# Performance work log

Hardware: AMD Instinct MI355X
Metric: run time of the kernel (lower is better)

Reference implementation:

```python
import jax, jax.numpy as jnp
import numpy as np

EMBED = 1024
HEADS = 16
HEAD_DIM = EMBED // HEADS
B, S = 2, 2048


def setup_inputs() -> dict:
    key = jax.random.key(0)
    ks = jax.random.split(key, 9)
    std = 1.0 / np.sqrt(EMBED)
    mk = lambda k: jax.random.uniform(k, (EMBED, EMBED), jnp.float32, -std, std)
    bk = lambda k: jax.random.uniform(k, (EMBED,), jnp.float32, -std, std)
    return {
        "x": jax.random.normal(ks[0], (B, S, EMBED), jnp.float32),
        "Wq": mk(ks[1]), "bq": bk(ks[2]),
        "Wk": mk(ks[3]), "bk": bk(ks[4]),
        "Wv": mk(ks[5]), "bv": bk(ks[6]),
        "Wo": mk(ks[7]), "bo": bk(ks[8]),
    }


def reference(x, Wq, bq, Wk, bk, Wv, bv, Wo, bo):
    b, s, _ = x.shape
    scale = HEAD_DIM ** -0.5
    # Linear layers: y = x @ W^T + b (torch nn.Linear convention)
    def heads(W, bias):
        y = jnp.einsum('bse,fe->bsf', x, W) + bias
        return y.reshape(b, s, HEADS, HEAD_DIM).transpose(0, 2, 1, 3)  # [b,h,s,d]
    Q, K, V = heads(Wq, bq), heads(Wk, bk), heads(Wv, bv)
    scores = jnp.einsum('bhqd,bhkd->bhqk', Q, K) * scale
    attn = jax.nn.softmax(scores, axis=-1)
    out = jnp.einsum('bhqk,bhkd->bhqd', attn, V)
    out = out.transpose(0, 2, 1, 3).reshape(b, s, EMBED)
    return jnp.einsum('bse,fe->bsf', out, Wo) + bo
```

## Files before the change

kernel.cpp:

```cpp
#include <hip/hip_runtime.h>
#include <hip/hip_bf16.h>
#include <cstddef>

#define SEQ   2048
#define EMB   1024
#define NHEAD 16
#define HDIM  64
#define BATCH 2
#define MROWS (BATCH * SEQ)
#define BH_STRIDE (SEQ * HDIM)
#define CSC_F 0.180336874f

typedef __attribute__((ext_vector_type(8))) short frag_ab;
typedef __attribute__((ext_vector_type(4))) float frag_cd;

#define GLOBAL_AS __attribute__((address_space(1)))
#define LDS_AS    __attribute__((address_space(3)))

__device__ __forceinline__ unsigned short f2bf(float f) {
    unsigned u = __float_as_uint(f);
    u += 0x7FFF + ((u >> 16) & 1);
    return (unsigned short)(u >> 16);
}
__device__ __forceinline__ unsigned short f2bf_trunc(float f) {
    return (unsigned short)(__float_as_uint(f) >> 16);
}
__device__ __forceinline__ void gld16(const unsigned short* g, unsigned short* l) {
    __builtin_amdgcn_global_load_lds((GLOBAL_AS const unsigned int*)g,
                                     (LDS_AS unsigned int*)l, 16, 0, 0);
}

__global__ __launch_bounds__(256) void cvt_all(const float* __restrict__ x,
                                               const float* __restrict__ Wq,
                                               const float* __restrict__ Wk,
                                               const float* __restrict__ Wv,
                                               unsigned short* __restrict__ xb,
                                               unsigned short* __restrict__ wqkv) {
    size_t e = ((size_t)blockIdx.x * 256 + threadIdx.x) * 8;
    const float* s;
    unsigned short* d;
    float sc = 1.0f;
    const size_t NX = (size_t)MROWS * EMB;
    const size_t NW = (size_t)EMB * EMB;
    if (e < NX) { s = x + e; d = xb + e; }
    else if (e < NX + NW)     { s = Wq + (e - NX);          d = wqkv + (e - NX); sc = CSC_F; }
    else if (e < NX + 2 * NW) { s = Wk + (e - NX - NW);     d = wqkv + (e - NX); }
    else                      { s = Wv + (e - NX - 2 * NW); d = wqkv + (e - NX); }
    float4 f0 = *(const float4*)s;
    float4 f1 = *(const float4*)(s + 4);
    ushort4 lo, hi;
    lo.x = f2bf(f0.x * sc); lo.y = f2bf(f0.y * sc); lo.z = f2bf(f0.z * sc); lo.w = f2bf(f0.w * sc);
    hi.x = f2bf(f1.x * sc); hi.y = f2bf(f1.y * sc); hi.z = f2bf(f1.z * sc); hi.w = f2bf(f1.w * sc);
    *(ushort4*)d = lo;
    *(ushort4*)(d + 4) = hi;
}

__global__ __launch_bounds__(256) void cvt_bf16(const float* __restrict__ s,
                                                unsigned short* __restrict__ d, int n) {
    int i = (blockIdx.x * 256 + threadIdx.x) * 8;
    if (i >= n) return;
    float4 f0 = *(const float4*)&s[i];
    float4 f1 = *(const float4*)&s[i + 4];
    ushort4 lo, hi;
    lo.x = f2bf(f0.x); lo.y = f2bf(f0.y); lo.z = f2bf(f0.z); lo.w = f2bf(f0.w);
    hi.x = f2bf(f1.x); hi.y = f2bf(f1.y); hi.z = f2bf(f1.z); hi.w = f2bf(f1.w);
    *(ushort4*)&d[i] = lo;
    *(ushort4*)&d[i + 4] = hi;
}

template <bool QKV>
__global__ __launch_bounds__(256, 3) void gemm128(const unsigned short* __restrict__ A,
                                                  const unsigned short* __restrict__ W0,
                                                  const unsigned short* __restrict__ W1,
                                                  const unsigned short* __restrict__ W2,
                                                  const float* __restrict__ b0,
                                                  const float* __restrict__ b1,
                                                  const float* __restrict__ b2,
                                                  void* __restrict__ o0,
                                                  void* __restrict__ o1,
                                                  void* __restrict__ o2) {
    constexpr int K = EMB;
    __shared__ __align__(16) unsigned short SB[16384];
    unsigned short* As = SB;
    unsigned short* Bs = SB + 8192;

    const int bidx = blockIdx.x;
    const int g8 = bidx & 7, t = bidx >> 3;
    const int my = g8 * 4 + (t & 3);
    const int mx = QKV ? ((t >> 2) & 7) : (t >> 2);
    const int z = QKV ? (t >> 5) : 0;

    const unsigned short* W = (z == 0) ? W0 : (z == 1) ? W1 : W2;
    const float* bias = (z == 0) ? b0 : (z == 1) ? b1 : b2;
    void* outv = (z == 0) ? o0 : (z == 1) ? o1 : o2;

    const int m0 = my * 128;
    const int n0 = mx * 128;
    const int tid = threadIdx.x;
    const int lane = tid & 63, w = tid >> 6;
    const int wr = w >> 1, wc = w & 1;
    const int lm = lane & 15, lq = lane >> 4;

    const int cs = (((tid & 7) ^ ((tid >> 3) & 7)) << 3);
    const int sx = lm & 7;

    frag_cd acc[4][4];
#pragma unroll
    for (int mt = 0; mt < 4; ++mt)
#pragma unroll
        for (int nt = 0; nt < 4; ++nt) acc[mt][nt] = (frag_cd){0.f, 0.f, 0.f, 0.f};

    for (int k0 = 0; k0 < K; k0 += 64) {
#pragma unroll
        for (int it = 0; it < 4; ++it) {
            int flat = (it * 256 + tid) * 8;
            int r = flat >> 6;
            gld16(&A[(size_t)(m0 + r) * K + k0 + cs], &As[flat]);
        }
#pragma unroll
        for (int it = 0; it < 4; ++it) {
            int flat = (it * 256 + tid) * 8;
            int r = flat >> 6;
            gld16(&W[(size_t)(n0 + r) * K + k0 + cs], &Bs[flat]);
        }
        __syncthreads();

#pragma unroll
        for (int kk = 0; kk < 2; ++kk) {
            frag_ab af[4], bf[4];
#pragma unroll
            for (int mt = 0; mt < 4; ++mt)
                af[mt] = *(const frag_ab*)&As[(wr * 64 + mt * 16 + lm) * 64
                                              + (((kk * 4 + lq) ^ sx) << 3)];
#pragma unroll
            for (int nt = 0; nt < 4; ++nt)
                bf[nt] = *(const frag_ab*)&Bs[(wc * 64 + nt * 16 + lm) * 64
                                              + (((kk * 4 + lq) ^ sx) << 3)];
#pragma unroll
            for (int mt = 0; mt < 4; ++mt)
#pragma unroll
                for (int nt = 0; nt < 4; ++nt)
                    acc[mt][nt] = __builtin_amdgcn_mfma_f32_16x16x32_bf16(
                        af[mt], bf[nt], acc[mt][nt], 0, 0, 0);
        }
        __syncthreads();
    }

    const float bscale = (QKV && z == 0) ? CSC_F : 1.0f;
    if (!QKV) {
#pragma unroll
        for (int mt = 0; mt < 4; ++mt)
#pragma unroll
            for (int nt = 0; nt < 4; ++nt) {
                int col = n0 + wc * 64 + nt * 16 + lm;
                float bv = bias[col];
#pragma unroll
                for (int r = 0; r < 4; ++r) {
                    int row = m0 + wr * 64 + mt * 16 + lq * 4 + r;
                    ((float*)outv)[(size_t)row * EMB + col] = acc[mt][nt][r] + bv;
                }
            }
    } else {
#pragma unroll
        for (int mt = 0; mt < 4; ++mt)
#pragma unroll
            for (int nt = 0; nt < 4; ++nt) {
                int col = n0 + wc * 64 + nt * 16 + lm;
                float bv = bias[col] * bscale;
#pragma unroll
                for (int r = 0; r < 4; ++r) {
                    unsigned short o = f2bf(acc[mt][nt][r] + bv);
                    int l, pos;
                    if (z < 2) {
                        l = wc * 16 + (wr * 4 + mt) * 2 + (nt >> 1);
                        pos = ((nt * 2 + (lm >> 3)) & 3) * 128 + (lq * 4 + r) * 8 + (lm & 7);
                    } else {
                        l = wc * 16 + (wr * 2 + (mt >> 1)) * 4 + nt;
                        pos = ((mt & 1) * 2 + (lq >> 1)) * 128 + lm * 8 + (lq & 1) * 4 + r;
                    }
                    SB[l * 512 + pos] = o;
                }
            }
        __syncthreads();

        unsigned short* out = (unsigned short*)outv;
        const int b = m0 >> 11;
        const int hb = n0 >> 6;
        const int sg16 = (m0 & (SEQ - 1)) >> 4;
        const int sb32 = (m0 & (SEQ - 1)) >> 5;
#pragma unroll
        for (int it = 0; it < 8; ++it) {
            int cl = it * 4 + w;
            uint4 v = *(const uint4*)&SB[cl * 512 + lane * 8];
            size_t chunk;
            if (z < 2) {
                int h = cl >> 4, sg = (cl >> 1) & 7, dh = cl & 1;
                chunk = ((size_t)(b * NHEAD + hb + h) * 128 + sg16 + sg) * 2 + dh;
            } else {
                int h = cl >> 4, sb = (cl >> 2) & 3, dq = cl & 3;
                chunk = ((size_t)(b * NHEAD + hb + h) * 64 + sb32 + sb) * 4 + dq;
            }
            *(uint4*)&out[chunk * 512 + lane * 8] = v;
        }
    }
}

#define PSTRIDE 72

struct KVset { frag_ab k[4][2]; frag_ab v[2][4]; };

__device__ __forceinline__ void kv_load(const unsigned short* __restrict__ Kb,
                                        const unsigned short* __restrict__ Vb,
                                        int j, int lane, KVset& s) {
    const int kg = j >> 4, jb = j >> 5;
#pragma unroll
    for (int c = 0; c < 4; ++c) {
        s.k[c][0] = *(const frag_ab*)&Kb[(((kg + c) * 2 + 0) * 64 + lane) * 8];
        s.k[c][1] = *(const frag_ab*)&Kb[(((kg + c) * 2 + 1) * 64 + lane) * 8];
    }
#pragma unroll
    for (int jj = 0; jj < 2; ++jj)
#pragma unroll
        for (int dt = 0; dt < 4; ++dt)
            s.v[jj][dt] = *(const frag_ab*)&Vb[(((jb + jj) * 4 + dt) * 64 + lane) * 8];
}

__device__ __forceinline__ void attn_step(const KVset& s, const frag_ab (&qf)[2][2],
                                          const frag_ab& vone,
                                          frag_cd (&oa)[2][4], frag_cd (&oc)[2],
                                          unsigned short* __restrict__ Pw,
                                          int lm, int lq) {
    const frag_cd z = (frag_cd){0.f, 0.f, 0.f, 0.f};
#pragma unroll
    for (int c = 0; c < 4; ++c) {
#pragma unroll
        for (int qi = 0; qi < 2; ++qi) {
            frag_cd sc = __builtin_amdgcn_mfma_f32_16x16x32_bf16(qf[qi][0], s.k[c][0], z, 0, 0, 0);
            sc = __builtin_amdgcn_mfma_f32_16x16x32_bf16(qf[qi][1], s.k[c][1], sc, 0, 0, 0);
#pragma unroll
            for (int r = 0; r < 4; ++r) {
                float p = __builtin_amdgcn_exp2f(sc[r]);
                Pw[(qi * 16 + lq * 4 + r) * PSTRIDE + c * 16 + lm] = f2bf_trunc(p);
            }
        }
    }

    frag_ab pf[2][2];
#pragma unroll
    for (int qi = 0; qi < 2; ++qi) {
        pf[qi][0] = *(const frag_ab*)&Pw[(qi * 16 + lm) * PSTRIDE + lq * 8];
        pf[qi][1] = *(const frag_ab*)&Pw[(qi * 16 + lm) * PSTRIDE + 32 + lq * 8];
        oc[qi] = __builtin_amdgcn_mfma_f32_16x16x32_bf16(pf[qi][0], vone, oc[qi], 0, 0, 0);
        oc[qi] = __builtin_amdgcn_mfma_f32_16x16x32_bf16(pf[qi][1], vone, oc[qi], 0, 0, 0);
    }

#pragma unroll
    for (int dt = 0; dt < 4; ++dt)
#pragma unroll
        for (int qi = 0; qi < 2; ++qi) {
            oa[qi][dt] = __builtin_amdgcn_mfma_f32_16x16x32_bf16(pf[qi][0], s.v[0][dt], oa[qi][dt], 0, 0, 0);
            oa[qi][dt] = __builtin_amdgcn_mfma_f32_16x16x32_bf16(pf[qi][1], s.v[1][dt], oa[qi][dt], 0, 0, 0);
        }
}

__global__ __launch_bounds__(256, 2) void attn_fused(const unsigned short* __restrict__ Q,
                                                     const unsigned short* __restrict__ Kf,
                                                     const unsigned short* __restrict__ Vf,
                                                     unsigned short* __restrict__ O) {
    const int bidx = blockIdx.x;
    const int g8 = bidx & 7, t = bidx >> 3;
    const int bh = g8 * 4 + (t & 3);
    const int qt = t >> 2;
    const int w = threadIdx.x >> 6, lane = threadIdx.x & 63;
    const int lm = lane & 15, lq = lane >> 4;

    __shared__ __align__(16) unsigned short P[4][32 * PSTRIDE];

    const unsigned short* Qb = Q + (size_t)bh * BH_STRIDE;
    const unsigned short* Kb = Kf + (size_t)bh * BH_STRIDE;
    const unsigned short* Vb = Vf + (size_t)bh * BH_STRIDE;

    const int ga = qt * 8 + w * 2;
    frag_ab qf[2][2];
#pragma unroll
    for (int qi = 0; qi < 2; ++qi) {
        qf[qi][0] = *(const frag_ab*)&Qb[(((ga + qi) * 2 + 0) * 64 + lane) * 8];
        qf[qi][1] = *(const frag_ab*)&Qb[(((ga + qi) * 2 + 1) * 64 + lane) * 8];
    }

    frag_ab vone;
#pragma unroll
    for (int j = 0; j < 8; ++j) vone[j] = (short)0x3F80;

    frag_cd oa[2][4], oc[2];
#pragma unroll
    for (int qi = 0; qi < 2; ++qi) {
        oc[qi] = (frag_cd){0.f, 0.f, 0.f, 0.f};
#pragma unroll
        for (int dt = 0; dt < 4; ++dt) oa[qi][dt] = (frag_cd){0.f, 0.f, 0.f, 0.f};
    }

    unsigned short* Pw = &P[w][0];

    KVset A, B;
    kv_load(Kb, Vb, 0, lane, A);
    for (int j0 = 0; j0 < SEQ; j0 += 128) {
        kv_load(Kb, Vb, (j0 + 64) & (SEQ - 1), lane, B);
        __builtin_amdgcn_sched_barrier(0);
        attn_step(A, qf, vone, oa, oc, Pw, lm, lq);
        kv_load(Kb, Vb, (j0 + 128) & (SEQ - 1), lane, A);
        __builtin_amdgcn_sched_barrier(0);
        attn_step(B, qf, vone, oa, oc, Pw, lm, lq);
    }

    const int b = bh >> 4, h = bh & (NHEAD - 1);
#pragma unroll
    for (int qi = 0; qi < 2; ++qi) {
        const int q0 = (ga + qi) * 16;
#pragma unroll
        for (int r = 0; r < 4; ++r) {
            float inv = 1.0f / oc[qi][r];
            int srow = q0 + lq * 4 + r;
#pragma unroll
            for (int dt = 0; dt < 4; ++dt) {
                int d = dt * 16 + lm;
                O[((size_t)(b * SEQ + srow)) * EMB + h * HDIM + d] = f2bf(oa[qi][dt][r] * inv);
            }
        }
    }
}

extern "C" void kernel_launch(void* const* d_in, const int* in_sizes, int n_in,
                              void* d_out, int out_size, void* d_ws, size_t ws_size,
                              hipStream_t stream) {
    const float* x  = (const float*)d_in[0];
    const float* Wq = (const float*)d_in[1];
    const float* bq = (const float*)d_in[2];
    const float* Wk = (const float*)d_in[3];
    const float* bk = (const float*)d_in[4];
    const float* Wv = (const float*)d_in[5];
    const float* bv = (const float*)d_in[6];
    const float* Wo = (const float*)d_in[7];
    const float* bo = (const float*)d_in[8];

    unsigned short* xb    = (unsigned short*)d_ws;
    unsigned short* q_ws  = xb + (size_t)MROWS * EMB;
    unsigned short* k_ws  = q_ws + (size_t)MROWS * EMB;
    unsigned short* vt_ws = k_ws + (size_t)MROWS * EMB;
    unsigned short* o_ws  = xb;
    unsigned short* wqkv  = (unsigned short*)d_out;
    unsigned short* wo_b  = q_ws;

    dim3 blk(256);
    cvt_all<<<dim3((MROWS * EMB + 3 * EMB * EMB) / 2048), blk, 0, stream>>>(
        x, Wq, Wk, Wv, xb, wqkv);

    gemm128<true><<<dim3(768), blk, 0, stream>>>(
        xb, wqkv, wqkv + EMB * EMB, wqkv + 2 * EMB * EMB,
        bq, bk, bv, q_ws, k_ws, vt_ws);

    attn_fused<<<dim3(512), blk, 0, stream>>>(q_ws, k_ws, vt_ws, o_ws);

    cvt_bf16<<<dim3(EMB * EMB / 2048), blk, 0, stream>>>(Wo, wo_b, EMB * EMB);
    gemm128<false><<<dim3(256), blk, 0, stream>>>(
        o_ws, wo_b, wo_b, wo_b, bo, bo, bo, d_out, d_out, d_out);
}
```

Baseline: 184.0 us.

## Split attention KV sequence across wave pairs with LDS reduction

Each block now handles 4 query tiles instead of 8. Its four waves form two query groups times two KV halves, and the grid doubles to 1024 blocks. Partial numerators and denominators from the second KV half go through LDS and are added by the first-half waves before normalisation and store. This raises parallelism and occupancy for the attention kernel, in exchange for extra LDS traffic, two block barriers, and idle waves during the epilogue. The softmax has no max-subtraction, so plain summation of the partials stays correct.

```diff
diff --git a/kernel.cpp b/kernel.cpp
--- a/kernel.cpp
+++ b/kernel.cpp
@@ -273,14 +273,17 @@
     const int qt = t >> 2;
     const int w = threadIdx.x >> 6, lane = threadIdx.x & 63;
     const int lm = lane & 15, lq = lane >> 4;
-
-    __shared__ __align__(16) unsigned short P[4][32 * PSTRIDE];
+    const int qs = w & 1;
+    const int kh = w >> 1;
+
+    __shared__ __align__(16) unsigned char SMEM[20480];
+    unsigned short* P = (unsigned short*)SMEM;
 
     const unsigned short* Qb = Q + (size_t)bh * BH_STRIDE;
     const unsigned short* Kb = Kf + (size_t)bh * BH_STRIDE;
     const unsigned short* Vb = Vf + (size_t)bh * BH_STRIDE;
 
-    const int ga = qt * 8 + w * 2;
+    const int ga = qt * 4 + qs * 2;
     frag_ab qf[2][2];
 #pragma unroll
     for (int qi = 0; qi < 2; ++qi) {
@@ -300,31 +303,67 @@
         for (int dt = 0; dt < 4; ++dt) oa[qi][dt] = (frag_cd){0.f, 0.f, 0.f, 0.f};
     }
 
-    unsigned short* Pw = &P[w][0];
+    unsigned short* Pw = &P[w * (32 * PSTRIDE)];
+    const int j_base = kh * (SEQ / 2);
+    const int KMASK = SEQ / 2 - 1;
 
     KVset A, B;
-    kv_load(Kb, Vb, 0, lane, A);
-    for (int j0 = 0; j0 < SEQ; j0 += 128) {
-        kv_load(Kb, Vb, (j0 + 64) & (SEQ - 1), lane, B);
+    kv_load(Kb, Vb, j_base, lane, A);
+    for (int jj = 0; jj < SEQ / 2; jj += 128) {
+        kv_load(Kb, Vb, j_base + ((jj + 64) & KMASK), lane, B);
         __builtin_amdgcn_sched_barrier(0);
         attn_step(A, qf, vone, oa, oc, Pw, lm, lq);
-        kv_load(Kb, Vb, (j0 + 128) & (SEQ - 1), lane, A);
+        kv_load(Kb, Vb, j_base + ((jj + 128) & KMASK), lane, A);
         __builtin_amdgcn_sched_barrier(0);
         attn_step(B, qf, vone, oa, oc, Pw, lm, lq);
     }
 
-    const int b = bh >> 4, h = bh & (NHEAD - 1);
-#pragma unroll
-    for (int qi = 0; qi < 2; ++qi) {
-        const int q0 = (ga + qi) * 16;
-#pragma unroll
-        for (int r = 0; r < 4; ++r) {
-            float inv = 1.0f / oc[qi][r];
-            int srow = q0 + lq * 4 + r;
-#pragma unroll
-            for (int dt = 0; dt < 4; ++dt) {
-                int d = dt * 16 + lm;
-                O[((size_t)(b * SEQ + srow)) * EMB + h * HDIM + d] = f2bf(oa[qi][dt][r] * inv);
+    float* R0 = (float*)SMEM;
+    float* R1 = R0 + 2560;
+
+    __syncthreads();
+    if (w >= 2) {
+        float* dst = (w == 2) ? R0 : R1;
+        int idx = 0;
+#pragma unroll
+        for (int qi = 0; qi < 2; ++qi)
+#pragma unroll
+            for (int dt = 0; dt < 4; ++dt)
+#pragma unroll
+                for (int r = 0; r < 4; ++r) { dst[idx * 64 + lane] = oa[qi][dt][r]; ++idx; }
+#pragma unroll
+        for (int qi = 0; qi < 2; ++qi)
+#pragma unroll
+            for (int r = 0; r < 4; ++r) { dst[idx * 64 + lane] = oc[qi][r]; ++idx; }
+    }
+    __syncthreads();
+    if (w < 2) {
+        const float* src = (w == 0) ? R0 : R1;
+        int idx = 0;
+#pragma unroll
+        for (int qi = 0; qi < 2; ++qi)
+#pragma unroll
+            for (int dt = 0; dt < 4; ++dt)
+#pragma unroll
+                for (int r = 0; r < 4; ++r) { oa[qi][dt][r] += src[idx * 64 + lane]; ++idx; }
+#pragma unroll
+        for (int qi = 0; qi < 2; ++qi)
+#pragma unroll
+            for (int r = 0; r < 4; ++r) { oc[qi][r] += src[idx * 64 + lane]; ++idx; }
+
+        const int b = bh >> 4, h = bh & (NHEAD - 1);
+#pragma unroll
+        for (int qi = 0; qi < 2; ++qi) {
+            const int q0 = (ga + qi) * 16;
+#pragma unroll
+            for (int r = 0; r < 4; ++r) {
+                float inv = 1.0f / oc[qi][r];
+                int srow = q0 + lq * 4 + r;
+#pragma unroll
+                for (int dt = 0; dt < 4; ++dt) {
+                    int d = dt * 16 + lm;
+                    O[((size_t)(b * SEQ + srow)) * EMB + h * HDIM + d] = f2bf(oa[qi][dt][r] * inv);
+                }
             }
         }
     }
@@ -359,7 +398,7 @@
         xb, wqkv, wqkv + EMB * EMB, wqkv + 2 * EMB * EMB,
         bq, bk, bv, q_ws, k_ws, vt_ws);
 
-    attn_fused<<<dim3(512), blk, 0, stream>>>(q_ws, k_ws, vt_ws, o_ws);
+    attn_fused<<<dim3(1024), blk, 0, stream>>>(q_ws, k_ws, vt_ws, o_ws);
 
     cvt_bf16<<<dim3(EMB * EMB / 2048), blk, 0, stream>>>(Wo, wo_b, EMB * EMB);
     gemm128<false><<<dim3(256), blk, 0, stream>>>(
```

New measurement: 188.9 us. 1.03x slower.
